# Kernel tuning notes

Hardware: AMD Instinct MI355X
Metric: run time of the kernel (lower is better)

## Reference

```python
import jax, jax.numpy as jnp
import numpy as np

B, T, N, H, E, LH, OUT, D = 64, 12, 325, 64, 32, 128, 12, 1
META_OFF = 65  # x[..., :1] is the signal, x[..., 65:] is the 32-dim temporal meta input


def _mlp(meta, W1, b1, W2, b2):
    # meta: (B,E); W1: (4,E,LH); W2: (4,LH,O) -> (4,B,O); 4 = gates g,i,f,o
    h = jax.nn.relu(jnp.einsum('be,geh->gbh', meta, W1) + b1[:, None, :])
    return jnp.einsum('gbh,gho->gbo', h, W2) + b2[:, None, :]


def setup_inputs() -> dict:
    key = jax.random.key(0)
    ks = jax.random.split(key, 16)
    s = lambda k, shape: jax.random.normal(k, shape, dtype=jnp.float32) * 0.05
    return {
        'x': jax.random.normal(ks[0], (B, T, N, 1 + 64 + E), dtype=jnp.float32),
        'lwx_W1': s(ks[1], (4, E, LH)), 'lwx_b1': s(ks[2], (4, LH)),
        'lwx_W2': s(ks[3], (4, LH, D * H)), 'lwx_b2': s(ks[4], (4, D * H)),
        'lwh_W1': s(ks[5], (4, E, LH)), 'lwh_b1': s(ks[6], (4, LH)),
        'lwh_W2': s(ks[7], (4, LH, H * H)), 'lwh_b2': s(ks[8], (4, H * H)),
        'lb_W1': s(ks[9], (4, E, LH)), 'lb_b1': s(ks[10], (4, LH)),
        'lb_W2': s(ks[11], (4, LH, H)), 'lb_b2': s(ks[12], (4, H)),
        'fc1_W': s(ks[13], (H, H // 2)), 'fc1_b': jnp.zeros((H // 2,), jnp.float32),
        'fc2_W': s(ks[14], (H // 2, OUT * D)), 'fc2_b': jnp.zeros((OUT * D,), jnp.float32),
    }


def reference(x, lwx_W1, lwx_b1, lwx_W2, lwx_b2,
              lwh_W1, lwh_b1, lwh_W2, lwh_b2,
              lb_W1, lb_b1, lb_W2, lb_b2,
              fc1_W, fc1_b, fc2_W, fc2_b):
    batch = x.shape[0]
    meta = jnp.mean(x[:, :, 0, META_OFF:], axis=1)  # (B,E)
    xs = jnp.transpose(x[..., :D], (1, 0, 2, 3))    # (T,B,N,D)

    Wx = _mlp(meta, lwx_W1, lwx_b1, lwx_W2, lwx_b2).reshape(4, batch, D, H)
    Wh = _mlp(meta, lwh_W1, lwh_b1, lwh_W2, lwh_b2).reshape(4, batch, H, H)
    b = _mlp(meta, lb_W1, lb_b1, lb_W2, lb_b2).reshape(4, batch, 1, H)

    def step(carry, xt):
        h, c = carry
        # (4,B,N,H): per-batch weights -> batched matmuls for all 4 gates
        z = (jnp.einsum('bnd,gbdh->gbnh', xt, Wx)
             + jnp.einsum('bnh,gbhk->gbnk', h, Wh) + b)
        g = jnp.tanh(z[0])
        i = jax.nn.sigmoid(z[1])
        f = jax.nn.sigmoid(z[2])
        o = jax.nn.sigmoid(z[3])
        c = g * i + c * f
        h = jnp.tanh(c) * o
        return (h, c), None

    # h0=c0=0 reproduces the torch t==0 special case exactly
    h0 = jnp.zeros((batch, N, H), x.dtype)
    (h, _), _ = jax.lax.scan(step, (h0, h0), xs)

    out = jax.nn.relu(h)
    out = jax.nn.relu(out @ fc1_W + fc1_b) @ fc2_W + fc2_b  # (B,N,OUT*D)
    out = out.reshape(batch, N, OUT, D)
    return jnp.transpose(out, (0, 2, 1, 3))  # (B,OUT,N,D)
```

## Files before the change

### kernel.cpp

```cpp
#include <hip/hip_runtime.h>
#include <stdint.h>

#define TT 12
#define NN 325
#define HH 64
#define EE 32
#define LHH 128
#define OO 12
#define CIN 97
#define MOFF 65
#define BB 64

typedef __attribute__((ext_vector_type(8))) short bf8;
typedef __attribute__((ext_vector_type(4))) float f4;

__device__ __forceinline__ float sigf(float x) {
  return __builtin_amdgcn_rcpf(1.f + __builtin_amdgcn_exp2f(-1.4426950408889634f * x));
}
__device__ __forceinline__ float tanhfast(float x) {
  return 1.f - 2.f * __builtin_amdgcn_rcpf(1.f + __builtin_amdgcn_exp2f(2.8853900817779268f * x));
}
__device__ __forceinline__ unsigned short f2bf(float f) {
  unsigned int u = __float_as_uint(f);
  u += 0x7fffu + ((u >> 16) & 1u);
  return (unsigned short)(u >> 16);
}
__device__ __forceinline__ float bf2f(unsigned short s) {
  return __uint_as_float(((unsigned int)s) << 16);
}

__global__ __launch_bounds__(256) void k_meta(
    const float* __restrict__ x,
    const float* __restrict__ xw1, const float* __restrict__ xb1,
    const float* __restrict__ xw2, const float* __restrict__ xb2,
    const float* __restrict__ hw1, const float* __restrict__ hb1,
    const float* __restrict__ bw1, const float* __restrict__ bb1,
    const float* __restrict__ bw2, const float* __restrict__ bb2,
    float* __restrict__ hid_ws, float* __restrict__ wx_ws,
    float* __restrict__ bg_ws)
{
  const int g = blockIdx.x >> 6, b = blockIdx.x & 63, tid = threadIdx.x;
  __shared__ float mpart[TT][EE];
  __shared__ float meta_s[EE];
  __shared__ float hid3[3][LHH];
  __shared__ float psum[2][4][HH];

  for (int idx = tid; idx < TT * EE; idx += 256) {
    const int t = idx >> 5, e = idx & 31;
    mpart[t][e] = x[(size_t)((b * TT + t) * NN) * CIN + MOFF + e];
  }
  __syncthreads();
  if (tid < EE) {
    float s = 0.f;
    #pragma unroll
    for (int t = 0; t < TT; ++t) s += mpart[t][tid];
    meta_s[tid] = s * (1.f / 12.f);
  }
  __syncthreads();

  for (int idx = tid; idx < 3 * LHH; idx += 256) {
    const int mlp = idx >> 7, l = idx & 127;
    const float* W1 = (mlp == 0) ? xw1 : ((mlp == 1) ? hw1 : bw1);
    const float* B1 = (mlp == 0) ? xb1 : ((mlp == 1) ? hb1 : bb1);
    float a = B1[g * LHH + l];
    const float* w = W1 + (size_t)g * (EE * LHH) + l;
    #pragma unroll
    for (int e = 0; e < EE; ++e) a = fmaf(meta_s[e], w[e * LHH], a);
    a = fmaxf(a, 0.f);
    hid3[mlp][l] = a;
    if (mlp == 1) hid_ws[g * (BB * LHH) + b * LHH + l] = a;
  }
  __syncthreads();

  {
    const int part = tid >> 6, h = tid & 63;
    float ax = 0.f, ab = 0.f;
    const float* wxp = xw2 + (size_t)g * (LHH * HH) + h;
    const float* wbp = bw2 + (size_t)g * (LHH * HH) + h;
    #pragma unroll
    for (int ll = 0; ll < 32; ++ll) {
      const int l = part * 32 + ll;
      ax = fmaf(hid3[0][l], wxp[l * HH], ax);
      ab = fmaf(hid3[2][l], wbp[l * HH], ab);
    }
    psum[0][part][h] = ax;
    psum[1][part][h] = ab;
  }
  __syncthreads();
  if (tid < 128) {
    const int isb = tid >> 6, h = tid & 63;
    const float bias = (isb ? bb2 : xb2)[g * HH + h];
    const float a = bias + psum[isb][0][h] + psum[isb][1][h]
                         + psum[isb][2][h] + psum[isb][3][h];
    (isb ? bg_ws : wx_ws)[b * 256 + g * 64 + h] = a;
  }
}

__global__ __launch_bounds__(256) void k_wh(
    const float* __restrict__ x,
    const float* __restrict__ hw2, const float* __restrict__ hb2,
    const float* __restrict__ hid_ws, unsigned short* __restrict__ whb,
    float* __restrict__ xg)
{
  const int g = blockIdx.x >> 8, i = (blockIdx.x >> 2) & 63, bq = blockIdx.x & 3;
  const int tid = threadIdx.x;
  __shared__ float hs[16][132];
  __shared__ float w2s[LHH][HH];

  {
    const int flat = blockIdx.x * 244 + tid;
    if (tid < 244 && flat < BB * TT * NN) {
      const int b = flat / (TT * NN);
      const int r = flat - b * (TT * NN);
      const int t = r / NN;
      const int n = r - t * NN;
      xg[flat] = x[(size_t)((b * TT + t) * NN + n) * CIN];
    }
  }

  for (int idx = tid; idx < 16 * LHH; idx += 256)
    hs[idx >> 7][idx & 127] =
        hid_ws[g * (BB * LHH) + (bq * 16 + (idx >> 7)) * LHH + (idx & 127)];
  for (int idx = tid; idx < LHH * HH; idx += 256)
    w2s[idx >> 6][idx & 63] =
        hw2[(size_t)(g * LHH + (idx >> 6)) * 4096 + i * 64 + (idx & 63)];
  __syncthreads();

  const int r0 = (tid >> 5) * 2, j0 = (tid & 31) * 2;
  float acc[2][2] = {};
  for (int l = 0; l < LHH; l += 4) {
    const f4 h0 = *(const f4*)&hs[r0][l];
    const f4 h1 = *(const f4*)&hs[r0 + 1][l];
    #pragma unroll
    for (int ll = 0; ll < 4; ++ll) {
      const float w0 = w2s[l + ll][j0];
      const float w1 = w2s[l + ll][j0 + 1];
      acc[0][0] = fmaf(h0[ll], w0, acc[0][0]);
      acc[0][1] = fmaf(h0[ll], w1, acc[0][1]);
      acc[1][0] = fmaf(h1[ll], w0, acc[1][0]);
      acc[1][1] = fmaf(h1[ll], w1, acc[1][1]);
    }
  }

  const int kh = i >> 5, quad = (i >> 3) & 3, j8 = i & 7;
  #pragma unroll
  for (int rr = 0; rr < 2; ++rr) {
    const int b = bq * 16 + r0 + rr;
    #pragma unroll
    for (int jj = 0; jj < 2; ++jj) {
      const int j = j0 + jj;
      const float v = acc[rr][jj] + hb2[g * 4096 + i * 64 + j];
      const int col = g * 64 + j;
      const int nt = col >> 4, c16 = col & 15;
      const int lane = quad * 16 + c16;
      whb[(size_t)((b * 32 + kh * 16 + nt) * 64 + lane) * 8 + j8] = f2bf(v);
    }
  }
}

__global__ __launch_bounds__(256, 3) void k_lstm(
    const float* __restrict__ xg, const float* __restrict__ wx_ws,
    const float* __restrict__ bg_ws, const unsigned short* __restrict__ whb,
    const float* __restrict__ fc1W, const float* __restrict__ fc1b,
    const float* __restrict__ fc2W, const float* __restrict__ fc2b,
    float* __restrict__ out)
{
  const int rb = blockIdx.x, b = blockIdx.y, tid = threadIdx.x;
  const int wave = tid >> 6, lane = tid & 63, quad = lane >> 4, c16 = lane & 15;
  const int n0 = rb * 32;

  __shared__ __align__(16) unsigned short Hs[2][2][16][72];
  __shared__ float Xs[TT][32];
  __shared__ float fc1s[HH * 32];
  __shared__ float fc2s[32 * OO];
  __shared__ float HIDs[32][36];
  __shared__ float fc1bs[32];
  __shared__ float fc2bs[OO];

  for (int idx = tid; idx < TT * 32; idx += 256) {
    const int t = idx >> 5, r = idx & 31, n = n0 + r;
    Xs[t][r] = (n < NN) ? xg[b * (TT * NN) + t * NN + n] : 0.f;
  }
  for (int idx = tid; idx < HH * 32; idx += 256) fc1s[idx] = fc1W[idx];
  for (int idx = tid; idx < 32 * OO; idx += 256) fc2s[idx] = fc2W[idx];
  if (tid < 32) fc1bs[tid] = fc1b[tid];
  if (tid < OO) fc2bs[tid] = fc2b[tid];

  float wxv[4], bgv[4];
  #pragma unroll
  for (int g = 0; g < 4; ++g) {
    wxv[g] = wx_ws[b * 256 + g * 64 + wave * 16 + c16];
    bgv[g] = bg_ws[b * 256 + g * 64 + wave * 16 + c16];
  }
  bf8 wf[2][4];
  #pragma unroll
  for (int kh = 0; kh < 2; ++kh)
    #pragma unroll
    for (int g = 0; g < 4; ++g)
      wf[kh][g] = *(const bf8*)(whb + (size_t)((b * 32 + kh * 16 + g * 4 + wave) * 64 + lane) * 8);

  float cst[2][4];
  #pragma unroll
  for (int ta = 0; ta < 2; ++ta)
    #pragma unroll
    for (int r = 0; r < 4; ++r) cst[ta][r] = 0.f;

  __syncthreads();

  #pragma unroll 1
  for (int t = 0; t < TT; ++t) {
    bf8 af[2][2];
    if (t > 0) {
      #pragma unroll
      for (int ta = 0; ta < 2; ++ta) {
        af[ta][0] = *(const bf8*)&Hs[(t - 1) & 1][ta][c16][quad * 8];
        af[ta][1] = *(const bf8*)&Hs[(t - 1) & 1][ta][c16][32 + quad * 8];
      }
    }
    f4 ac[2][4];
    #pragma unroll
    for (int ta = 0; ta < 2; ++ta) {
      float xr[4];
      #pragma unroll
      for (int r = 0; r < 4; ++r) xr[r] = Xs[t][ta * 16 + quad * 4 + r];
      #pragma unroll
      for (int g = 0; g < 4; ++g)
        #pragma unroll
        for (int r = 0; r < 4; ++r)
          ac[ta][g][r] = fmaf(xr[r], wxv[g], bgv[g]);
    }
    if (t > 0) {
      #pragma unroll
      for (int ta = 0; ta < 2; ++ta)
        #pragma unroll
        for (int g = 0; g < 4; ++g) {
          ac[ta][g] = __builtin_amdgcn_mfma_f32_16x16x32_bf16(af[ta][0], wf[0][g], ac[ta][g], 0, 0, 0);
          ac[ta][g] = __builtin_amdgcn_mfma_f32_16x16x32_bf16(af[ta][1], wf[1][g], ac[ta][g], 0, 0, 0);
        }
    }
    #pragma unroll
    for (int ta = 0; ta < 2; ++ta)
      #pragma unroll
      for (int r = 0; r < 4; ++r) {
        const float gg = tanhfast(ac[ta][0][r]);
        const float ii = sigf(ac[ta][1][r]);
        const float ff = sigf(ac[ta][2][r]);
        const float oo = sigf(ac[ta][3][r]);
        const float cc = fmaf(gg, ii, cst[ta][r] * ff);
        cst[ta][r] = cc;
        const float hh = tanhfast(cc) * oo;
        Hs[t & 1][ta][quad * 4 + r][wave * 16 + c16] = f2bf(hh);
      }
    __syncthreads();
  }

  {
    const int row32 = tid & 31, uu = tid >> 5;
    const int ta = row32 >> 4, row = row32 & 15;
    float hacc[4];
    #pragma unroll
    for (int j = 0; j < 4; ++j) hacc[j] = fc1bs[uu * 4 + j];
    #pragma unroll
    for (int kc = 0; kc < 8; ++kc) {
      const bf8 hv = *(const bf8*)&Hs[1][ta][row][kc * 8];
      #pragma unroll
      for (int j8 = 0; j8 < 8; ++j8) {
        const float hk = fmaxf(bf2f((unsigned short)hv[j8]), 0.f);
        const int k = kc * 8 + j8;
        #pragma unroll
        for (int j = 0; j < 4; ++j)
          hacc[j] = fmaf(hk, fc1s[k * 32 + uu * 4 + j], hacc[j]);
      }
    }
    #pragma unroll
    for (int j = 0; j < 4; ++j)
      HIDs[row32][uu * 4 + j] = fmaxf(hacc[j], 0.f);
  }
  __syncthreads();
  for (int idx = tid; idx < 32 * OO; idx += 256) {
    const int o = idx >> 5, row32 = idx & 31;
    float a = fc2bs[o];
    #pragma unroll
    for (int k = 0; k < 32; ++k)
      a = fmaf(HIDs[row32][k], fc2s[k * OO + o], a);
    const int n = n0 + row32;
    if (n < NN)
      out[b * (OO * NN) + o * NN + n] = a;
  }
}

extern "C" void kernel_launch(void* const* d_in, const int* in_sizes, int n_in,
                              void* d_out, int out_size, void* d_ws, size_t ws_size,
                              hipStream_t stream) {
  const float* x    = (const float*)d_in[0];
  const float* xw1  = (const float*)d_in[1];
  const float* xb1  = (const float*)d_in[2];
  const float* xw2  = (const float*)d_in[3];
  const float* xb2  = (const float*)d_in[4];
  const float* hw1  = (const float*)d_in[5];
  const float* hb1  = (const float*)d_in[6];
  const float* hw2  = (const float*)d_in[7];
  const float* hb2  = (const float*)d_in[8];
  const float* bw1  = (const float*)d_in[9];
  const float* bb1  = (const float*)d_in[10];
  const float* bw2  = (const float*)d_in[11];
  const float* bb2  = (const float*)d_in[12];
  const float* fc1W = (const float*)d_in[13];
  const float* fc1b = (const float*)d_in[14];
  const float* fc2W = (const float*)d_in[15];
  const float* fc2b = (const float*)d_in[16];
  float* out = (float*)d_out;

  float* ws = (float*)d_ws;
  float* hid_ws = ws;
  float* wx_ws  = ws + 32768;
  float* bg_ws  = ws + 49152;
  float* xg_ws  = ws + 65536;
  unsigned short* whb = (unsigned short*)(ws + 65536 + BB * TT * NN);

  k_meta<<<256, 256, 0, stream>>>(x, xw1, xb1, xw2, xb2, hw1, hb1, bw1, bb1,
                                  bw2, bb2, hid_ws, wx_ws, bg_ws);
  k_wh<<<1024, 256, 0, stream>>>(x, hw2, hb2, hid_ws, whb, xg_ws);
  k_lstm<<<dim3(11, 64), 256, 0, stream>>>(xg_ws, wx_ws, bg_ws, whb,
                                           fc1W, fc1b, fc2W, fc2b, out);
}
```

Baseline: 214.5 us.

## Fuse meta MLP into Wh generation kernel and read x directly in LSTM

Merges the k_meta and k_wh kernels into a single k_prep kernel. Each block recomputes the meta mean and the first MLP layer for its 16 batches, and a subset of blocks also computes the Wx and bias MLPs. The separate xg gather is removed, so the LSTM kernel reads the signal channel straight from x. This drops one launch and the hid_ws and xg round trips through memory, at the cost of redundant meta and hidden-layer computation in every block.

```diff
diff --git a/kernel.cpp b/kernel.cpp
--- a/kernel.cpp
+++ b/kernel.cpp
@@ -29,137 +29,114 @@
   return __uint_as_float(((unsigned int)s) << 16);
 }
 
-__global__ __launch_bounds__(256) void k_meta(
+__global__ __launch_bounds__(256) void k_prep(
     const float* __restrict__ x,
     const float* __restrict__ xw1, const float* __restrict__ xb1,
     const float* __restrict__ xw2, const float* __restrict__ xb2,
     const float* __restrict__ hw1, const float* __restrict__ hb1,
+    const float* __restrict__ hw2, const float* __restrict__ hb2,
     const float* __restrict__ bw1, const float* __restrict__ bb1,
     const float* __restrict__ bw2, const float* __restrict__ bb2,
-    float* __restrict__ hid_ws, float* __restrict__ wx_ws,
-    float* __restrict__ bg_ws)
-{
-  const int g = blockIdx.x >> 6, b = blockIdx.x & 63, tid = threadIdx.x;
-  __shared__ float mpart[TT][EE];
-  __shared__ float meta_s[EE];
-  __shared__ float hid3[3][LHH];
-  __shared__ float psum[2][4][HH];
-
-  for (int idx = tid; idx < TT * EE; idx += 256) {
-    const int t = idx >> 5, e = idx & 31;
-    mpart[t][e] = x[(size_t)((b * TT + t) * NN) * CIN + MOFF + e];
-  }
-  __syncthreads();
-  if (tid < EE) {
-    float s = 0.f;
-    #pragma unroll
-    for (int t = 0; t < TT; ++t) s += mpart[t][tid];
-    meta_s[tid] = s * (1.f / 12.f);
-  }
-  __syncthreads();
-
-  for (int idx = tid; idx < 3 * LHH; idx += 256) {
-    const int mlp = idx >> 7, l = idx & 127;
-    const float* W1 = (mlp == 0) ? xw1 : ((mlp == 1) ? hw1 : bw1);
-    const float* B1 = (mlp == 0) ? xb1 : ((mlp == 1) ? hb1 : bb1);
-    float a = B1[g * LHH + l];
-    const float* w = W1 + (size_t)g * (EE * LHH) + l;
-    #pragma unroll
-    for (int e = 0; e < EE; ++e) a = fmaf(meta_s[e], w[e * LHH], a);
-    a = fmaxf(a, 0.f);
-    hid3[mlp][l] = a;
-    if (mlp == 1) hid_ws[g * (BB * LHH) + b * LHH + l] = a;
-  }
-  __syncthreads();
-
-  {
-    const int part = tid >> 6, h = tid & 63;
-    float ax = 0.f, ab = 0.f;
-    const float* wxp = xw2 + (size_t)g * (LHH * HH) + h;
-    const float* wbp = bw2 + (size_t)g * (LHH * HH) + h;
-    #pragma unroll
-    for (int ll = 0; ll < 32; ++ll) {
-      const int l = part * 32 + ll;
-      ax = fmaf(hid3[0][l], wxp[l * HH], ax);
-      ab = fmaf(hid3[2][l], wbp[l * HH], ab);
-    }
-    psum[0][part][h] = ax;
-    psum[1][part][h] = ab;
-  }
-  __syncthreads();
-  if (tid < 128) {
-    const int isb = tid >> 6, h = tid & 63;
-    const float bias = (isb ? bb2 : xb2)[g * HH + h];
-    const float a = bias + psum[isb][0][h] + psum[isb][1][h]
-                         + psum[isb][2][h] + psum[isb][3][h];
-    (isb ? bg_ws : wx_ws)[b * 256 + g * 64 + h] = a;
-  }
-}
-
-__global__ __launch_bounds__(256) void k_wh(
-    const float* __restrict__ x,
-    const float* __restrict__ hw2, const float* __restrict__ hb2,
-    const float* __restrict__ hid_ws, unsigned short* __restrict__ whb,
-    float* __restrict__ xg)
+    unsigned short* __restrict__ whb,
+    float* __restrict__ wx_ws, float* __restrict__ bg_ws)
 {
   const int g = blockIdx.x >> 8, i = (blockIdx.x >> 2) & 63, bq = blockIdx.x & 3;
   const int tid = threadIdx.x;
+  __shared__ float meta_s[16][EE];
   __shared__ float hs[16][132];
   __shared__ float w2s[LHH][HH];
 
-  {
-    const int flat = blockIdx.x * 244 + tid;
-    if (tid < 244 && flat < BB * TT * NN) {
-      const int b = flat / (TT * NN);
-      const int r = flat - b * (TT * NN);
-      const int t = r / NN;
-      const int n = r - t * NN;
-      xg[flat] = x[(size_t)((b * TT + t) * NN + n) * CIN];
-    }
-  }
-
-  for (int idx = tid; idx < 16 * LHH; idx += 256)
-    hs[idx >> 7][idx & 127] =
-        hid_ws[g * (BB * LHH) + (bq * 16 + (idx >> 7)) * LHH + (idx & 127)];
+  #pragma unroll
+  for (int k = 0; k < 2; ++k) {
+    const int idx = tid + 256 * k;
+    const int b16 = idx >> 5, e = idx & 31;
+    const int b = bq * 16 + b16;
+    float s = 0.f;
+    #pragma unroll
+    for (int t = 0; t < TT; ++t)
+      s += x[(size_t)((b * TT + t) * NN) * CIN + MOFF + e];
+    meta_s[b16][e] = s * (1.f / 12.f);
+  }
+  __syncthreads();
+
+  for (int idx = tid; idx < 16 * LHH; idx += 256) {
+    const int b16 = idx >> 7, l = idx & 127;
+    float a = hb1[g * LHH + l];
+    const float* w = hw1 + (size_t)g * (EE * LHH) + l;
+    #pragma unroll
+    for (int e = 0; e < EE; ++e) a = fmaf(meta_s[b16][e], w[e * LHH], a);
+    hs[b16][l] = fmaxf(a, 0.f);
+  }
   for (int idx = tid; idx < LHH * HH; idx += 256)
     w2s[idx >> 6][idx & 63] =
         hw2[(size_t)(g * LHH + (idx >> 6)) * 4096 + i * 64 + (idx & 63)];
   __syncthreads();
 
-  const int r0 = (tid >> 5) * 2, j0 = (tid & 31) * 2;
-  float acc[2][2] = {};
-  for (int l = 0; l < LHH; l += 4) {
-    const f4 h0 = *(const f4*)&hs[r0][l];
-    const f4 h1 = *(const f4*)&hs[r0 + 1][l];
-    #pragma unroll
-    for (int ll = 0; ll < 4; ++ll) {
-      const float w0 = w2s[l + ll][j0];
-      const float w1 = w2s[l + ll][j0 + 1];
-      acc[0][0] = fmaf(h0[ll], w0, acc[0][0]);
-      acc[0][1] = fmaf(h0[ll], w1, acc[0][1]);
-      acc[1][0] = fmaf(h1[ll], w0, acc[1][0]);
-      acc[1][1] = fmaf(h1[ll], w1, acc[1][1]);
-    }
-  }
-
-  const int kh = i >> 5, quad = (i >> 3) & 3, j8 = i & 7;
-  #pragma unroll
-  for (int rr = 0; rr < 2; ++rr) {
-    const int b = bq * 16 + r0 + rr;
-    #pragma unroll
-    for (int jj = 0; jj < 2; ++jj) {
-      const int j = j0 + jj;
-      const float v = acc[rr][jj] + hb2[g * 4096 + i * 64 + j];
-      const int col = g * 64 + j;
-      const int nt = col >> 4, c16 = col & 15;
-      const int lane = quad * 16 + c16;
-      whb[(size_t)((b * 32 + kh * 16 + nt) * 64 + lane) * 8 + j8] = f2bf(v);
+  {
+    const int r0 = (tid >> 5) * 2, j0 = (tid & 31) * 2;
+    float acc[2][2] = {};
+    for (int l = 0; l < LHH; l += 4) {
+      const f4 h0 = *(const f4*)&hs[r0][l];
+      const f4 h1 = *(const f4*)&hs[r0 + 1][l];
+      #pragma unroll
+      for (int ll = 0; ll < 4; ++ll) {
+        const float w0 = w2s[l + ll][j0];
+        const float w1 = w2s[l + ll][j0 + 1];
+        acc[0][0] = fmaf(h0[ll], w0, acc[0][0]);
+        acc[0][1] = fmaf(h0[ll], w1, acc[0][1]);
+        acc[1][0] = fmaf(h1[ll], w0, acc[1][0]);
+        acc[1][1] = fmaf(h1[ll], w1, acc[1][1]);
+      }
+    }
+
+    const int kh = i >> 5, quad = (i >> 3) & 3, j8 = i & 7;
+    #pragma unroll
+    for (int rr = 0; rr < 2; ++rr) {
+      const int b = bq * 16 + r0 + rr;
+      #pragma unroll
+      for (int jj = 0; jj < 2; ++jj) {
+        const int j = j0 + jj;
+        const float v = acc[rr][jj] + hb2[g * 4096 + i * 64 + j];
+        const int col = g * 64 + j;
+        const int nt = col >> 4, c16 = col & 15;
+        const int lane = quad * 16 + c16;
+        whb[(size_t)((b * 32 + kh * 16 + nt) * 64 + lane) * 8 + j8] = f2bf(v);
+      }
+    }
+  }
+
+  if (i < 2) {
+    const float* W1 = i ? bw1 : xw1;
+    const float* B1 = i ? bb1 : xb1;
+    const float* W2 = i ? bw2 : xw2;
+    const float* B2 = i ? bb2 : xb2;
+    float* dst = i ? bg_ws : wx_ws;
+    __syncthreads();
+    for (int idx = tid; idx < 16 * LHH; idx += 256) {
+      const int b16 = idx >> 7, l = idx & 127;
+      float a = B1[g * LHH + l];
+      const float* w = W1 + (size_t)g * (EE * LHH) + l;
+      #pragma unroll
+      for (int e = 0; e < EE; ++e) a = fmaf(meta_s[b16][e], w[e * LHH], a);
+      hs[b16][l] = fmaxf(a, 0.f);
+    }
+    for (int idx = tid; idx < LHH * HH; idx += 256)
+      w2s[idx >> 6][idx & 63] =
+          W2[(size_t)(g * LHH + (idx >> 6)) * HH + (idx & 63)];
+    __syncthreads();
+    for (int idx = tid; idx < 16 * HH; idx += 256) {
+      const int b16 = idx >> 6, h = idx & 63;
+      float a = B2[g * HH + h];
+      #pragma unroll 4
+      for (int l = 0; l < LHH; ++l)
+        a = fmaf(hs[b16][l], w2s[l][h], a);
+      dst[(bq * 16 + b16) * 256 + g * 64 + h] = a;
     }
   }
 }
 
 __global__ __launch_bounds__(256, 3) void k_lstm(
-    const float* __restrict__ xg, const float* __restrict__ wx_ws,
+    const float* __restrict__ x, const float* __restrict__ wx_ws,
     const float* __restrict__ bg_ws, const unsigned short* __restrict__ whb,
     const float* __restrict__ fc1W, const float* __restrict__ fc1b,
     const float* __restrict__ fc2W, const float* __restrict__ fc2b,
@@ -179,7 +156,7 @@
 
   for (int idx = tid; idx < TT * 32; idx += 256) {
     const int t = idx >> 5, r = idx & 31, n = n0 + r;
-    Xs[t][r] = (n < NN) ? xg[b * (TT * NN) + t * NN + n] : 0.f;
+    Xs[t][r] = (n < NN) ? x[(size_t)((b * TT + t) * NN + n) * CIN] : 0.f;
   }
   for (int idx = tid; idx < HH * 32; idx += 256) fc1s[idx] = fc1W[idx];
   for (int idx = tid; idx < 32 * OO; idx += 256) fc2s[idx] = fc2W[idx];
@@ -312,15 +289,12 @@
   float* out = (float*)d_out;
 
   float* ws = (float*)d_ws;
-  float* hid_ws = ws;
-  float* wx_ws  = ws + 32768;
-  float* bg_ws  = ws + 49152;
-  float* xg_ws  = ws + 65536;
-  unsigned short* whb = (unsigned short*)(ws + 65536 + BB * TT * NN);
-
-  k_meta<<<256, 256, 0, stream>>>(x, xw1, xb1, xw2, xb2, hw1, hb1, bw1, bb1,
-                                  bw2, bb2, hid_ws, wx_ws, bg_ws);
-  k_wh<<<1024, 256, 0, stream>>>(x, hw2, hb2, hid_ws, whb, xg_ws);
-  k_lstm<<<dim3(11, 64), 256, 0, stream>>>(xg_ws, wx_ws, bg_ws, whb,
+  float* wx_ws = ws;
+  float* bg_ws = ws + 16384;
+  unsigned short* whb = (unsigned short*)(ws + 32768);
+
+  k_prep<<<1024, 256, 0, stream>>>(x, xw1, xb1, xw2, xb2, hw1, hb1, hw2, hb2,
+                                   bw1, bb1, bw2, bb2, whb, wx_ws, bg_ws);
+  k_lstm<<<dim3(11, 64), 256, 0, stream>>>(x, wx_ws, bg_ws, whb,
                                            fc1W, fc1b, fc2W, fc2b, out);
 }
```

New measurement: 219.4 us. 1.02x slower.
